# Kernel tuning notes

Hardware: AMD Instinct MI355X
Metric: run time of the kernel (lower is better)

Reference implementation:

```python
import jax, jax.numpy as jnp
import numpy as np

N, D, K = 8192, 256, 64
NEG = -1e9


def setup_inputs() -> dict:
    key = jax.random.key(0)
    ks = jax.random.split(key, 4)
    s = 1.0 / np.sqrt(D)
    return {
        "example_features": jax.random.normal(ks[0], (N, D), dtype=jnp.float32),
        "Wq": jax.random.normal(ks[1], (D, D), dtype=jnp.float32) * s,
        "bq": jnp.zeros((D,), dtype=jnp.float32),
        "Wk": jax.random.normal(ks[2], (D, D), dtype=jnp.float32) * s,
        "bk": jnp.zeros((D,), dtype=jnp.float32),
        "Wv": jax.random.normal(ks[3], (D, D), dtype=jnp.float32) * s,
        "bv": jnp.zeros((D,), dtype=jnp.float32),
        "temperature": jnp.ones((1,), dtype=jnp.float32),
        "k": K,
    }


def reference(example_features, Wq, bq, Wk, bk, Wv, bv, temperature, k):
    n, d = example_features.shape
    # QKV projections (torch Linear: x @ W.T + b)
    Q = example_features @ Wq.T + bq
    Km = example_features @ Wk.T + bk
    V = example_features @ Wv.T + bv
    # dense scores with learned temperature
    scores = (Q @ Km.T) / (temperature[0] * jnp.sqrt(jnp.float32(d)))
    # self-exclusion mask on the diagonal
    idx = jnp.arange(n)
    scores = scores.at[idx, idx].set(NEG)
    # per-row top-k thresholding (k < N-1 in this config)
    topk_vals = jax.lax.top_k(scores, k)[0]          # (N, k)
    threshold = topk_vals[:, -1:]                     # kth largest per row
    scores = jnp.where(scores < threshold, NEG, scores)
    attn = jax.nn.softmax(scores, axis=1)
    return attn @ V
```

## Files before the change

kernel.cpp:

```cpp
#include <hip/hip_runtime.h>
#include <math.h>

#define NN 8192
#define DD 256
#define TOPK 64
#define CAP 96
#define CCAP 256
#define CRMAX 2048
#define NEGVAL (-1000000000.0f)

typedef _Float16 f16;
typedef f16  f16x4 __attribute__((ext_vector_type(4)));
typedef f16  f16x8 __attribute__((ext_vector_type(8)));
typedef float f32x4 __attribute__((ext_vector_type(4)));

__global__ __launch_bounds__(256)
void gemm_qkv(const float* __restrict__ X,
              const float* __restrict__ Wq, const float* __restrict__ bq,
              const float* __restrict__ Wk, const float* __restrict__ bk,
              const float* __restrict__ Wv, const float* __restrict__ bv,
              f16* __restrict__ Qs, f16* __restrict__ Ks,
              float* __restrict__ Vf)
{
  __shared__ float As[32][68];
  __shared__ float Bs[3][32][68];
  const int t  = threadIdx.x;
  const int tm = t & 15;
  const int tn = t >> 4;
  const int m0 = blockIdx.x * 64;
  const int n0 = blockIdx.y * 64;

  float acc[3][4][4];
#pragma unroll
  for (int g = 0; g < 3; ++g)
#pragma unroll
    for (int i = 0; i < 4; ++i)
#pragma unroll
      for (int j = 0; j < 4; ++j) acc[g][i][j] = 0.0f;

  for (int k0 = 0; k0 < DD; k0 += 32) {
    __syncthreads();
#pragma unroll
    for (int i = 0; i < 2; ++i) {
      const int slot = t + i * 256;
      const int row  = slot >> 3;
      const int c4   = (slot & 7) << 2;
      float4 av = *(const float4*)(X + (size_t)(m0 + row) * DD + k0 + c4);
      As[c4 + 0][row] = av.x; As[c4 + 1][row] = av.y;
      As[c4 + 2][row] = av.z; As[c4 + 3][row] = av.w;
      float4 q4 = *(const float4*)(Wq + (size_t)(n0 + row) * DD + k0 + c4);
      Bs[0][c4 + 0][row] = q4.x; Bs[0][c4 + 1][row] = q4.y;
      Bs[0][c4 + 2][row] = q4.z; Bs[0][c4 + 3][row] = q4.w;
      float4 k4 = *(const float4*)(Wk + (size_t)(n0 + row) * DD + k0 + c4);
      Bs[1][c4 + 0][row] = k4.x; Bs[1][c4 + 1][row] = k4.y;
      Bs[1][c4 + 2][row] = k4.z; Bs[1][c4 + 3][row] = k4.w;
      float4 v4 = *(const float4*)(Wv + (size_t)(n0 + row) * DD + k0 + c4);
      Bs[2][c4 + 0][row] = v4.x; Bs[2][c4 + 1][row] = v4.y;
      Bs[2][c4 + 2][row] = v4.z; Bs[2][c4 + 3][row] = v4.w;
    }
    __syncthreads();
#pragma unroll
    for (int kk = 0; kk < 32; ++kk) {
      float a[4];
      *(float4*)&a[0] = *(const float4*)&As[kk][tm * 4];
      float b0[4], b1[4], b2[4];
      *(float4*)&b0[0] = *(const float4*)&Bs[0][kk][tn * 4];
      *(float4*)&b1[0] = *(const float4*)&Bs[1][kk][tn * 4];
      *(float4*)&b2[0] = *(const float4*)&Bs[2][kk][tn * 4];
#pragma unroll
      for (int i = 0; i < 4; ++i)
#pragma unroll
        for (int j = 0; j < 4; ++j) {
          acc[0][i][j] = fmaf(a[i], b0[j], acc[0][i][j]);
          acc[1][i][j] = fmaf(a[i], b1[j], acc[1][i][j]);
          acc[2][i][j] = fmaf(a[i], b2[j], acc[2][i][j]);
        }
    }
  }

#pragma unroll
  for (int r = 0; r < 4; ++r) {
    const int grow  = m0 + tm * 4 + r;
    const int gcol0 = n0 + tn * 4;
    {
      f16x4 h4, l4;
#pragma unroll
      for (int c = 0; c < 4; ++c) {
        const float val = acc[0][r][c] + bq[gcol0 + c];
        f16 h = (f16)val;
        h4[c] = h;
        l4[c] = (f16)(val - (float)h);
      }
      f16* base = Qs + (size_t)grow * 768 + gcol0;
      *(f16x4*)(base)       = h4;
      *(f16x4*)(base + 256) = h4;
      *(f16x4*)(base + 512) = l4;
    }
    {
      f16x4 h4, l4;
#pragma unroll
      for (int c = 0; c < 4; ++c) {
        const float val = acc[1][r][c] + bk[gcol0 + c];
        f16 h = (f16)val;
        h4[c] = h;
        l4[c] = (f16)(val - (float)h);
      }
      f16* base = Ks + (size_t)grow * 768 + gcol0;
      *(f16x4*)(base)       = h4;
      *(f16x4*)(base + 256) = l4;
      *(f16x4*)(base + 512) = h4;
    }
    {
      float val[4];
#pragma unroll
      for (int c = 0; c < 4; ++c)
        val[c] = acc[2][r][c] + bv[gcol0 + c];
      *(float4*)(Vf + (size_t)grow * DD + gcol0) =
          make_float4(val[0], val[1], val[2], val[3]);
    }
  }
}

typedef __attribute__((address_space(1))) const void GV;
typedef __attribute__((address_space(3))) void LV;
__device__ __forceinline__ void gl_lds16(const void* g, void* l) {
  __builtin_amdgcn_global_load_lds((GV*)g, (LV*)l, 16, 0, 0);
}

__global__ __launch_bounds__(512, 1)
void gemm_scores_f16(const f16* __restrict__ Aq, const f16* __restrict__ Bk,
                     float* __restrict__ C, const float* __restrict__ temp,
                     int rowOff)
{
  __shared__ __align__(16) f16 lds[2][2][256 * 64];

  const int t  = threadIdx.x;
  const int l  = t & 63;
  const int w  = t >> 6;
  const int wm = w >> 2;
  const int wn = w & 3;
  const int m0 = blockIdx.x * 256;
  const int n0 = blockIdx.y * 256;
  const int fr = l & 15;
  const int fg = l >> 4;

  const int srow = w * 8 + (l >> 3);
  const int koff = ((l & 7) ^ (l >> 3)) * 8;

  f32x4 acc[8][4];
#pragma unroll
  for (int m = 0; m < 8; ++m)
#pragma unroll
    for (int n = 0; n < 4; ++n) acc[m][n] = (f32x4){0.f, 0.f, 0.f, 0.f};

  auto stage = [&](int d, int kt) {
    const int kb = kt * 64 + koff;
#pragma unroll
    for (int j = 0; j < 4; ++j)
      gl_lds16(Aq + (size_t)(m0 + j * 64 + srow) * 768 + kb,
               &lds[d][0][j * 4096 + w * 512]);
#pragma unroll
    for (int j = 0; j < 4; ++j)
      gl_lds16(Bk + (size_t)(n0 + j * 64 + srow) * 768 + kb,
               &lds[d][1][j * 4096 + w * 512]);
  };

  stage(0, 0);

#pragma unroll 1
  for (int kt = 0; kt < 12; ++kt) {
    const int d = kt & 1;
    if (kt + 1 < 12) {
      stage(d ^ 1, kt + 1);
      asm volatile("s_waitcnt vmcnt(8)" ::: "memory");
    } else {
      asm volatile("s_waitcnt vmcnt(0)" ::: "memory");
    }
    __builtin_amdgcn_s_barrier();
    __builtin_amdgcn_sched_barrier(0);

    const f16* Ab = &lds[d][0][0];
    const f16* Bb = &lds[d][1][0];
#pragma unroll
    for (int kk = 0; kk < 2; ++kk) {
      const int g = ((kk * 4 + fg) ^ (fr & 7)) * 8;
      f16x8 bf[4];
#pragma unroll
      for (int n = 0; n < 4; ++n)
        bf[n] = *(const f16x8*)&Bb[(wn * 64 + n * 16 + fr) * 64 + g];
#pragma unroll
      for (int mh = 0; mh < 2; ++mh) {
        f16x8 af[4];
#pragma unroll
        for (int i = 0; i < 4; ++i)
          af[i] = *(const f16x8*)&Ab[(wm * 128 + (mh * 4 + i) * 16 + fr) * 64 + g];
        __builtin_amdgcn_s_setprio(1);
#pragma unroll
        for (int i = 0; i < 4; ++i)
#pragma unroll
          for (int n = 0; n < 4; ++n)
            acc[mh * 4 + i][n] = __builtin_amdgcn_mfma_f32_16x16x32_f16(
                af[i], bf[n], acc[mh * 4 + i][n], 0, 0, 0);
        __builtin_amdgcn_s_setprio(0);
      }
    }
    __builtin_amdgcn_sched_barrier(0);
    __builtin_amdgcn_s_barrier();
  }

  const float invts = 1.0f / (temp[0] * 16.0f);
#pragma unroll
  for (int m = 0; m < 8; ++m)
#pragma unroll
    for (int n = 0; n < 4; ++n) {
      const int gcol = n0 + wn * 64 + n * 16 + fr;
#pragma unroll
      for (int j = 0; j < 4; ++j) {
        const int lrow = m0 + wm * 128 + m * 16 + fg * 4 + j;
        float x = acc[m][n][j] * invts;
        if (rowOff + lrow == gcol) x = NEGVAL;
        C[(size_t)lrow * NN + gcol] = x;
      }
    }
}

__global__ __launch_bounds__(256)
void topk_softmax4(const float* __restrict__ Sc, int rowOff,
                   float* __restrict__ wts, int* __restrict__ idx,
                   int* __restrict__ cnt)
{
  __shared__ unsigned hist[256];
  __shared__ float    candv[CCAP];
  __shared__ int      candi[CCAP];
  __shared__ float    pb[CAP];
  __shared__ int      jb[CAP];
  __shared__ float    wmax[4], wsum[4];
  __shared__ int      wtot[4];
  __shared__ int      sB;
  __shared__ unsigned uT;

  const int t = threadIdx.x;
  const int l = t & 63;
  const int w = t >> 6;
  const int grow = rowOff + blockIdx.x;
  const float* srow = Sc + (size_t)blockIdx.x * NN;

  float v[32];
#pragma unroll
  for (int c = 0; c < 8; ++c) {
    float4 f = *(const float4*)(srow + ((size_t)c * 256 + t) * 4);
    v[c * 4 + 0] = f.x; v[c * 4 + 1] = f.y; v[c * 4 + 2] = f.z; v[c * 4 + 3] = f.w;
  }

  float lm = -3.0e38f;
#pragma unroll
  for (int r = 0; r < 32; ++r) lm = fmaxf(lm, v[r]);
#pragma unroll
  for (int off = 32; off; off >>= 1) lm = fmaxf(lm, __shfl_xor(lm, off));
  if (l == 0) wmax[w] = lm;
  __syncthreads();
  const float m = fmaxf(fmaxf(wmax[0], wmax[1]), fmaxf(wmax[2], wmax[3]));

  float lo = m - 2.5f;
  float invw = 0.0f;
  int B = -1;
  for (int iter = 0; iter < 8; ++iter) {
    hist[t] = 0u;
    __syncthreads();
    invw = 256.0f / (m - lo);
#pragma unroll
    for (int r = 0; r < 32; ++r) {
      float s = v[r];
      if (s >= lo) {
        int b = (int)((s - lo) * invw);
        b = (b > 255) ? 255 : b;
        atomicAdd(&hist[b], 1u);
      }
    }
    __syncthreads();
    const int c = (int)hist[t];
    int x = c;
#pragma unroll
    for (int off = 1; off < 64; off <<= 1) {
      int y = __shfl_down(x, off);
      if (l + off < 64) x += y;
    }
    if (l == 0) wtot[w] = x;
    __syncthreads();
    int hi = 0;
#pragma unroll
    for (int ww = 0; ww < 4; ++ww) if (ww > w) hi += wtot[ww];
    const int S = x + hi;
    const int total = wtot[0] + wtot[1] + wtot[2] + wtot[3];
    if (total >= TOPK) {
      if (S >= TOPK && S - c < TOPK) sB = t;
      __syncthreads();
      B = sB;
      break;
    }
    __syncthreads();
    lo = m - 2.5f * (float)(2 << iter);
  }
  if (B < 0) B = 0;

  int cc = 0;
#pragma unroll
  for (int r = 0; r < 32; ++r) {
    float s = v[r];
    if (s >= lo) {
      int b = (int)((s - lo) * invw);
      b = (b > 255) ? 255 : b;
      if (b >= B) ++cc;
    }
  }
  int x = cc;
#pragma unroll
  for (int off = 1; off < 64; off <<= 1) {
    int y = __shfl_up(x, off);
    if (l >= off) x += y;
  }
  if (l == 63) wtot[w] = x;
  __syncthreads();
  int lowsum = 0;
#pragma unroll
  for (int ww = 0; ww < 4; ++ww) if (ww < w) lowsum += wtot[ww];
  int base = lowsum + x - cc;
  const int ctotal = wtot[0] + wtot[1] + wtot[2] + wtot[3];
#pragma unroll
  for (int r = 0; r < 32; ++r) {
    float s = v[r];
    if (s >= lo) {
      int b = (int)((s - lo) * invw);
      b = (b > 255) ? 255 : b;
      if (b >= B) {
        if (base < CCAP) {
          candv[base] = s;
          candi[base] = ((r >> 2) * 256 + t) * 4 + (r & 3);
        }
        ++base;
      }
    }
  }
  __syncthreads();
  const int L = (ctotal < CCAP) ? ctotal : CCAP;

  if (t == 0) uT = 0xFFFFFFFFu;
  __syncthreads();
  if (t < L) {
    float vi = candv[t];
    int g = 0;
    for (int j = 0; j < L; ++j) g += (candv[j] > vi) ? 1 : 0;
    if (g <= TOPK - 1) {
      unsigned ub = __float_as_uint(vi);
      unsigned u = (ub & 0x80000000u) ? ~ub : (ub | 0x80000000u);
      atomicMin(&uT, u);
    }
  }
  __syncthreads();
  const unsigned uth = uT;
  const float T = __uint_as_float((uth & 0x80000000u) ? (uth & 0x7FFFFFFFu) : ~uth);

  const bool keep = (t < L) && (candv[t] >= T);
  const unsigned long long bal = __ballot(keep);
  if (l == 0) wtot[w] = __popcll(bal);
  __syncthreads();
  int lowsum2 = 0;
#pragma unroll
  for (int ww = 0; ww < 4; ++ww) if (ww < w) lowsum2 += wtot[ww];
  const int pos = lowsum2 + __popcll(bal & ((1ULL << l) - 1ULL));
  const int total2 = wtot[0] + wtot[1] + wtot[2] + wtot[3];
  if (keep && pos < CAP) {
    pb[pos] = __expf(candv[t] - m);
    jb[pos] = candi[t];
  }
  __syncthreads();
  const int L2 = (total2 < CAP) ? total2 : CAP;

  float ps = 0.0f;
  for (int i = t; i < L2; i += 256) ps += pb[i];
#pragma unroll
  for (int off = 32; off; off >>= 1) ps += __shfl_xor(ps, off);
  if (l == 0) wsum[w] = ps;
  __syncthreads();
  const float inv = 1.0f / (wsum[0] + wsum[1] + wsum[2] + wsum[3]);
  for (int i = t; i < L2; i += 256) {
    wts[(size_t)grow * CAP + i] = pb[i] * inv;
    idx[(size_t)grow * CAP + i] = jb[i];
  }
  if (t == 0) cnt[grow] = L2;
}

__global__ __launch_bounds__(256)
void sparse_av(const float* __restrict__ V, const float* __restrict__ wts,
               const int* __restrict__ idx, const int* __restrict__ cnt,
               float* __restrict__ out)
{
  __shared__ float wl[CAP];
  __shared__ int   jl[CAP];
  const int t = threadIdx.x;
  const int row = blockIdx.x;
  const int L = cnt[row];
  if (t < CAP && t < L) {
    wl[t] = wts[(size_t)row * CAP + t];
    jl[t] = idx[(size_t)row * CAP + t];
  }
  __syncthreads();
  float acc = 0.0f;
  for (int i = 0; i < L; ++i)
    acc = fmaf(wl[i], V[(size_t)jl[i] * DD + t], acc);
  out[(size_t)row * DD + t] = acc;
}

extern "C" void kernel_launch(void* const* d_in, const int* in_sizes, int n_in,
                              void* d_out, int out_size, void* d_ws, size_t ws_size,
                              hipStream_t stream)
{
  const float* X    = (const float*)d_in[0];
  const float* Wq   = (const float*)d_in[1];
  const float* bq   = (const float*)d_in[2];
  const float* Wk   = (const float*)d_in[3];
  const float* bk   = (const float*)d_in[4];
  const float* Wv   = (const float*)d_in[5];
  const float* bv   = (const float*)d_in[6];
  const float* temp = (const float*)d_in[7];
  float* out = (float*)d_out;
  float* ws  = (float*)d_ws;

  const size_t avail = ws_size / sizeof(float);

  const size_t szV   = (size_t)NN * DD;
  const size_t szHL  = (size_t)NN * 768 / 2;
  const size_t szWts = (size_t)NN * CAP;
  const size_t szIdx = (size_t)NN * CAP;
  const size_t szCnt = NN;
  const size_t fixed = szV + 2 * szHL + szWts + szIdx + szCnt;

  size_t o = 0;
  float* Vbuf = ws + o; o += szV;
  f16*   Qs   = (f16*)(ws + o); o += szHL;
  f16*   Ks   = (f16*)(ws + o); o += szHL;
  float* wts  = ws + o; o += szWts;
  int*   idxb = (int*)(ws + o); o += szIdx;
  int*   cntb = (int*)(ws + o); o += szCnt;

  if (avail <= fixed + (size_t)256 * NN) return;
  int CR = (int)(((avail - fixed) / NN) / 256) * 256;
  if (CR > CRMAX) CR = CRMAX;
  if (CR > NN) CR = NN;
  float* Sc = ws + o;

  dim3 blk(256);
  dim3 blk2(512);

  gemm_qkv<<<dim3(NN/64, 4), blk, 0, stream>>>(X, Wq, bq, Wk, bk, Wv, bv,
                                               Qs, Ks, Vbuf);

  for (int r0 = 0; r0 < NN; r0 += CR) {
    const int rows = (NN - r0 < CR) ? (NN - r0) : CR;
    gemm_scores_f16<<<dim3(rows/256, NN/256), blk2, 0, stream>>>(
        Qs + (size_t)r0 * 768, Ks, Sc, temp, r0);
    topk_softmax4<<<dim3(rows), blk, 0, stream>>>(Sc, r0, wts, idxb, cntb);
  }

  sparse_av<<<dim3(NN), blk, 0, stream>>>(Vbuf, wts, idxb, cntb, out);
}
```

Before: 317.7 us.

## Deepen scores GEMM pipeline to four stages with 32-wide K tiles

Changes the scores GEMM's global-to-LDS staging from a double buffer of 64-wide K tiles to a four-slot ring of 32-wide K tiles, with three tiles in flight. Adds a new XOR swizzle for the narrower rows and adjusts the vmcnt waits to match. The goal is to hide more global-load latency behind the MFMA work. The trade-off is twice as many loop iterations and barriers, each doing half the MFMA work.

```diff
diff --git a/kernel.cpp b/kernel.cpp
--- a/kernel.cpp
+++ b/kernel.cpp
@@ -132,7 +132,7 @@
                      float* __restrict__ C, const float* __restrict__ temp,
                      int rowOff)
 {
-  __shared__ __align__(16) f16 lds[2][2][256 * 64];
+  __shared__ __align__(16) f16 lds[4][2][256 * 32];
 
   const int t  = threadIdx.x;
   const int l  = t & 63;
@@ -144,9 +144,6 @@
   const int fr = l & 15;
   const int fg = l >> 4;
 
-  const int srow = w * 8 + (l >> 3);
-  const int koff = ((l & 7) ^ (l >> 3)) * 8;
-
   f32x4 acc[8][4];
 #pragma unroll
   for (int m = 0; m < 8; ++m)
@@ -154,55 +151,55 @@
     for (int n = 0; n < 4; ++n) acc[m][n] = (f32x4){0.f, 0.f, 0.f, 0.f};
 
   auto stage = [&](int d, int kt) {
-    const int kb = kt * 64 + koff;
-#pragma unroll
-    for (int j = 0; j < 4; ++j)
-      gl_lds16(Aq + (size_t)(m0 + j * 64 + srow) * 768 + kb,
-               &lds[d][0][j * 4096 + w * 512]);
-#pragma unroll
-    for (int j = 0; j < 4; ++j)
-      gl_lds16(Bk + (size_t)(n0 + j * 64 + srow) * 768 + kb,
-               &lds[d][1][j * 4096 + w * 512]);
+    const int kb = kt * 32;
+#pragma unroll
+    for (int j = 0; j < 2; ++j) {
+      const int slot = j * 512 + t;
+      const int row  = slot >> 2;
+      const int sg   = (slot & 3) ^ (row & 3);
+      gl_lds16(Aq + (size_t)(m0 + row) * 768 + kb + sg * 8,
+               &lds[d][0][(j * 512 + w * 64) * 8]);
+      gl_lds16(Bk + (size_t)(n0 + row) * 768 + kb + sg * 8,
+               &lds[d][1][(j * 512 + w * 64) * 8]);
+    }
   };
 
   stage(0, 0);
+  stage(1, 1);
+  stage(2, 2);
 
 #pragma unroll 1
-  for (int kt = 0; kt < 12; ++kt) {
-    const int d = kt & 1;
-    if (kt + 1 < 12) {
-      stage(d ^ 1, kt + 1);
-      asm volatile("s_waitcnt vmcnt(8)" ::: "memory");
-    } else {
-      asm volatile("s_waitcnt vmcnt(0)" ::: "memory");
-    }
+  for (int kt = 0; kt < 24; ++kt) {
+    const int d = kt & 3;
+    if (kt + 3 < 24) stage((kt + 3) & 3, kt + 3);
+    if (kt <= 20)      asm volatile("s_waitcnt vmcnt(12)" ::: "memory");
+    else if (kt == 21) asm volatile("s_waitcnt vmcnt(8)"  ::: "memory");
+    else if (kt == 22) asm volatile("s_waitcnt vmcnt(4)"  ::: "memory");
+    else               asm volatile("s_waitcnt vmcnt(0)"  ::: "memory");
     __builtin_amdgcn_s_barrier();
     __builtin_amdgcn_sched_barrier(0);
 
     const f16* Ab = &lds[d][0][0];
     const f16* Bb = &lds[d][1][0];
-#pragma unroll
-    for (int kk = 0; kk < 2; ++kk) {
-      const int g = ((kk * 4 + fg) ^ (fr & 7)) * 8;
-      f16x8 bf[4];
-#pragma unroll
-      for (int n = 0; n < 4; ++n)
-        bf[n] = *(const f16x8*)&Bb[(wn * 64 + n * 16 + fr) * 64 + g];
-#pragma unroll
-      for (int mh = 0; mh < 2; ++mh) {
-        f16x8 af[4];
-#pragma unroll
-        for (int i = 0; i < 4; ++i)
-          af[i] = *(const f16x8*)&Ab[(wm * 128 + (mh * 4 + i) * 16 + fr) * 64 + g];
-        __builtin_amdgcn_s_setprio(1);
-#pragma unroll
-        for (int i = 0; i < 4; ++i)
-#pragma unroll
-          for (int n = 0; n < 4; ++n)
-            acc[mh * 4 + i][n] = __builtin_amdgcn_mfma_f32_16x16x32_f16(
-                af[i], bf[n], acc[mh * 4 + i][n], 0, 0, 0);
-        __builtin_amdgcn_s_setprio(0);
-      }
+    const int g = (fg ^ (fr & 3)) * 8;
+    f16x8 bf[4];
+#pragma unroll
+    for (int n = 0; n < 4; ++n)
+      bf[n] = *(const f16x8*)&Bb[(wn * 64 + n * 16 + fr) * 32 + g];
+#pragma unroll
+    for (int mh = 0; mh < 2; ++mh) {
+      f16x8 af[4];
+#pragma unroll
+      for (int i = 0; i < 4; ++i)
+        af[i] = *(const f16x8*)&Ab[(wm * 128 + (mh * 4 + i) * 16 + fr) * 32 + g];
+      __builtin_amdgcn_s_setprio(1);
+#pragma unroll
+      for (int i = 0; i < 4; ++i)
+#pragma unroll
+        for (int n = 0; n < 4; ++n)
+          acc[mh * 4 + i][n] = __builtin_amdgcn_mfma_f32_16x16x32_f16(
+              af[i], bf[n], acc[mh * 4 + i][n], 0, 0, 0);
+      __builtin_amdgcn_s_setprio(0);
     }
     __builtin_amdgcn_sched_barrier(0);
     __builtin_amdgcn_s_barrier();
```

Result: slower. 329.2 us (+3.6%).
